# Kernel tuning notes

Measured on AMD Instinct MI355X. Metric: run time of the kernel, lower is better.

## Reference

```python
import jax, jax.numpy as jnp
import numpy as np

B, T, C, H = 2, 2048, 1024, 16
HD = C // H  # head dim = 64


def setup_inputs() -> dict:
    key = jax.random.key(0)
    k1, k2, k3 = jax.random.split(key, 3)
    x = jax.random.normal(k1, (B, T, C), dtype=jnp.float32)
    W_attn = jax.random.normal(k2, (C, 3 * C), dtype=jnp.float32) * (C ** -0.5)
    W_proj = jax.random.normal(k3, (C, C), dtype=jnp.float32) * (C ** -0.5)
    b_proj = jnp.zeros((C,), dtype=jnp.float32)
    return {"x": x, "W_attn": W_attn, "W_proj": W_proj, "b_proj": b_proj}


def reference(x, W_attn, W_proj, b_proj):
    Bv, Tv, Cv = x.shape
    qkv = x @ W_attn  # [B, T, 3C]  (no bias: config.bias=False)
    # NOTE: source splits as k, q, v (k first!)
    k, q, v = jnp.split(qkv, 3, axis=2)
    # [B, H, T, HD]
    q = q.reshape(Bv, Tv, H, HD).transpose(0, 2, 1, 3)
    k = k.reshape(Bv, Tv, H, HD).transpose(0, 2, 1, 3)
    v = v.reshape(Bv, Tv, H, HD).transpose(0, 2, 1, 3)
    wei = jnp.einsum('bhqd,bhkd->bhqk', q, k) * (HD ** -0.5)
    causal = jnp.tril(jnp.ones((Tv, Tv), dtype=bool))
    wei = jnp.where(causal, wei, -jnp.inf)
    wei = jax.nn.softmax(wei, axis=-1)
    # dropout = 0.0 (eval) -> identity
    out = jnp.einsum('bhqk,bhkd->bhqd', wei, v)
    out = out.transpose(0, 2, 1, 3).reshape(Bv, Tv, Cv)
    out = out @ W_proj + b_proj
    return out
```

## Files before the change

### kernel.cpp

```cpp
#include <hip/hip_runtime.h>

typedef __attribute__((ext_vector_type(8))) short short8;
typedef __attribute__((ext_vector_type(4))) short short4v;
typedef __attribute__((ext_vector_type(4))) float float4v;

#define T_SEQ 2048
#define CDIM 1024
#define NHEAD 16
#define HDIM 64
#define LROW 40
#define PROW 72

__device__ __forceinline__ unsigned short f2bf(float f) {
    unsigned u = __builtin_bit_cast(unsigned, f);
    u += 0x7FFF + ((u >> 16) & 1);
    return (unsigned short)(u >> 16);
}

__global__ __launch_bounds__(256) void convert_f32_bf16_vec(
    const float* __restrict__ in, unsigned short* __restrict__ out) {
    int i = blockIdx.x * 256 + threadIdx.x;
    float4 v = ((const float4*)in)[i];
    ushort4 o;
    o.x = f2bf(v.x); o.y = f2bf(v.y); o.z = f2bf(v.z); o.w = f2bf(v.w);
    ((ushort4*)out)[i] = o;
}

__global__ __launch_bounds__(256) void transpose_f32_bf16(
    const float* __restrict__ in, unsigned short* __restrict__ out, int K, int N) {
    __shared__ float tile[32][33];
    int kb = blockIdx.x * 32, nb = blockIdx.y * 32;
    int tx = threadIdx.x & 31, ty = threadIdx.x >> 5;
    for (int r = 0; r < 4; r++)
        tile[ty + r * 8][tx] = in[(size_t)(kb + ty + r * 8) * N + nb + tx];
    __syncthreads();
    for (int r = 0; r < 4; r++)
        out[(size_t)(nb + ty + r * 8) * K + kb + tx] = f2bf(tile[tx][ty + r * 8]);
}

__global__ __launch_bounds__(256) void gemm_qkv(
    const unsigned short* __restrict__ A, const unsigned short* __restrict__ Bt,
    unsigned short* __restrict__ dK, unsigned short* __restrict__ dQ,
    unsigned short* __restrict__ dV) {
    const int K = 1024;
    const int NITER = K / 32;
    __shared__ unsigned short sA[2][128 * LROW];
    __shared__ unsigned short sB[2][128 * LROW];
    int tid = threadIdx.x, wave = tid >> 6, lane = tid & 63;
    int quad = lane >> 4, l16 = lane & 15;
    int wm = wave >> 1, wn = wave & 1;
    int blockM = blockIdx.y * 128, blockN = blockIdx.x * 128;
    int rlane = lane >> 2, seg = lane & 3;
    bool swapAB = (blockN >= 2048);

    const unsigned short* gA = A + (size_t)blockM * K;
    const unsigned short* gB = Bt + (size_t)blockN * K;

    float4v acc[4][4] = {};
    uint4 ra[2], rb[2];

    int srow[2], soff[2];
    for (int i = 0; i < 2; i++) {
        srow[i] = wave * 32 + i * 16 + rlane;
        soff[i] = srow[i] * LROW + seg * 8;
    }

    for (int i = 0; i < 2; i++) {
        ra[i] = *(const uint4*)(gA + (size_t)srow[i] * K + seg * 8);
        rb[i] = *(const uint4*)(gB + (size_t)srow[i] * K + seg * 8);
    }
    for (int i = 0; i < 2; i++) {
        *(uint4*)(sA[0] + soff[i]) = ra[i];
        *(uint4*)(sB[0] + soff[i]) = rb[i];
    }

    int aoff = (wm * 64 + l16) * LROW + quad * 8;
    int boff = (wn * 64 + l16) * LROW + quad * 8;

    for (int it = 0; it < NITER; it++) {
        int cur = it & 1;
        __syncthreads();
        if (it + 1 < NITER) {
            int kb = (it + 1) * 32;
            for (int i = 0; i < 2; i++) {
                ra[i] = *(const uint4*)(gA + (size_t)srow[i] * K + kb + seg * 8);
                rb[i] = *(const uint4*)(gB + (size_t)srow[i] * K + kb + seg * 8);
            }
        }
        const unsigned short* cA = sA[cur];
        const unsigned short* cB = sB[cur];
        short8 af[4], bf[4];
        for (int i = 0; i < 4; i++)
            af[i] = *(const short8*)(cA + aoff + i * 16 * LROW);
        for (int j = 0; j < 4; j++)
            bf[j] = *(const short8*)(cB + boff + j * 16 * LROW);
        if (!swapAB) {
            for (int i = 0; i < 4; i++)
                for (int j = 0; j < 4; j++)
                    acc[i][j] = __builtin_amdgcn_mfma_f32_16x16x32_bf16(
                        af[i], bf[j], acc[i][j], 0, 0, 0);
        } else {
            for (int i = 0; i < 4; i++)
                for (int j = 0; j < 4; j++)
                    acc[i][j] = __builtin_amdgcn_mfma_f32_16x16x32_bf16(
                        bf[j], af[i], acc[i][j], 0, 0, 0);
        }
        if (it + 1 < NITER) {
            int nxt = cur ^ 1;
            for (int i = 0; i < 2; i++) {
                *(uint4*)(sA[nxt] + soff[i]) = ra[i];
                *(uint4*)(sB[nxt] + soff[i]) = rb[i];
            }
        }
    }

    if (!swapAB) {
        const float QSCL = 0.18033688011112042f;
        for (int i = 0; i < 4; i++)
            for (int j = 0; j < 4; j++)
                for (int r = 0; r < 4; r++) {
                    int m = blockM + wm * 64 + i * 16 + quad * 4 + r;
                    int n = blockN + wn * 64 + j * 16 + l16;
                    int part = n >> 10, c = n & 1023;
                    int h = c >> 6, d = c & 63;
                    int bb = m >> 11, t = m & 2047;
                    int bh = bb * NHEAD + h;
                    if (part == 0) {
                        dK[(((size_t)bh * T_SEQ + t) << 6) + d] = f2bf(acc[i][j][r]);
                    } else {
                        dQ[(((size_t)bh * T_SEQ + t) << 6) + d] =
                            f2bf(acc[i][j][r] * QSCL);
                    }
                }
    } else {
        for (int i = 0; i < 4; i++)
            for (int j = 0; j < 4; j++)
                for (int r = 0; r < 4; r++) {
                    int n = blockN + wn * 64 + j * 16 + quad * 4 + r;
                    int m = blockM + wm * 64 + i * 16 + l16;
                    int c = n & 1023;
                    int h = c >> 6, d = c & 63;
                    int bb = m >> 11, t = m & 2047;
                    int bh = bb * NHEAD + h;
                    dV[((size_t)bh * HDIM + d) * T_SEQ + t] = f2bf(acc[i][j][r]);
                }
    }
}

__global__ __launch_bounds__(256) void gemm_proj(
    const unsigned short* __restrict__ A, const unsigned short* __restrict__ Bt,
    const float* __restrict__ bias, float* __restrict__ out) {
    const int K = 1024;
    const int NITER = K / 64;
    __shared__ unsigned short sA[2][64 * PROW];
    __shared__ unsigned short sB[2][64 * PROW];
    int tid = threadIdx.x, wave = tid >> 6, lane = tid & 63;
    int quad = lane >> 4, l16 = lane & 15;
    int wm = wave >> 1, wn = wave & 1;
    int blockM = blockIdx.y * 64, blockN = blockIdx.x * 64;

    int srow = tid >> 3;
    int sseg = tid & 7;
    const unsigned short* gA0 = A + (size_t)(blockM + srow) * K + sseg * 8;
    const unsigned short* gA1 = gA0 + (size_t)32 * K;
    const unsigned short* gB0 = Bt + (size_t)(blockN + srow) * K + sseg * 8;
    const unsigned short* gB1 = gB0 + (size_t)32 * K;
    int so0 = srow * PROW + sseg * 8;
    int so1 = (srow + 32) * PROW + sseg * 8;

    float4v acc[2][2] = {};
    uint4 ra0, ra1, rb0, rb1;

    ra0 = *(const uint4*)gA0; ra1 = *(const uint4*)gA1;
    rb0 = *(const uint4*)gB0; rb1 = *(const uint4*)gB1;
    *(uint4*)(sA[0] + so0) = ra0;
    *(uint4*)(sA[0] + so1) = ra1;
    *(uint4*)(sB[0] + so0) = rb0;
    *(uint4*)(sB[0] + so1) = rb1;

    int aoff = (wm * 32 + l16) * PROW + quad * 8;
    int boff = (wn * 32 + l16) * PROW + quad * 8;

    for (int it = 0; it < NITER; it++) {
        int cur = it & 1;
        __syncthreads();
        if (it + 1 < NITER) {
            int kb = (it + 1) * 64;
            ra0 = *(const uint4*)(gA0 + kb); ra1 = *(const uint4*)(gA1 + kb);
            rb0 = *(const uint4*)(gB0 + kb); rb1 = *(const uint4*)(gB1 + kb);
        }
        const unsigned short* cA = sA[cur];
        const unsigned short* cB = sB[cur];
        short8 af[2][2], bf[2][2];
        for (int i = 0; i < 2; i++)
            for (int k = 0; k < 2; k++)
                af[i][k] = *(const short8*)(cA + aoff + i * 16 * PROW + k * 32);
        for (int j = 0; j < 2; j++)
            for (int k = 0; k < 2; k++)
                bf[j][k] = *(const short8*)(cB + boff + j * 16 * PROW + k * 32);
        for (int i = 0; i < 2; i++)
            for (int j = 0; j < 2; j++) {
                acc[i][j] = __builtin_amdgcn_mfma_f32_16x16x32_bf16(
                    af[i][0], bf[j][0], acc[i][j], 0, 0, 0);
                acc[i][j] = __builtin_amdgcn_mfma_f32_16x16x32_bf16(
                    af[i][1], bf[j][1], acc[i][j], 0, 0, 0);
            }
        if (it + 1 < NITER) {
            int nxt = cur ^ 1;
            *(uint4*)(sA[nxt] + so0) = ra0;
            *(uint4*)(sA[nxt] + so1) = ra1;
            *(uint4*)(sB[nxt] + so0) = rb0;
            *(uint4*)(sB[nxt] + so1) = rb1;
        }
    }

    for (int i = 0; i < 2; i++)
        for (int j = 0; j < 2; j++)
            for (int r = 0; r < 4; r++) {
                int m = blockM + wm * 32 + i * 16 + quad * 4 + r;
                int n = blockN + wn * 32 + j * 16 + l16;
                out[(size_t)m * CDIM + n] = acc[i][j][r] + bias[n];
            }
}

__global__ __launch_bounds__(256) void attn_fwd(
    const unsigned short* __restrict__ Qp, const unsigned short* __restrict__ Kp,
    const unsigned short* __restrict__ Vt, unsigned short* __restrict__ att) {
    __shared__ unsigned short sK[2][64 * 72];
    __shared__ unsigned short sV[2][64 * 72];
    int tid = threadIdx.x, wave = tid >> 6, lane = tid & 63;
    int quad = lane >> 4, l16 = lane & 15;
    int bh = blockIdx.x;
    int bb = bh >> 4, h = bh & 15;
    size_t baseQ = (size_t)bh * T_SEQ * HDIM;
    size_t baseV = (size_t)bh * HDIM * T_SEQ;
    int row4 = tid >> 2, seg = tid & 3;

    int xt = 31 - blockIdx.y;
    int qb = xt * 64;
    int qrow = qb + wave * 16 + l16;

    const unsigned short* qr = Qp + baseQ + (size_t)qrow * HDIM;
    short8 qf0 = *(const short8*)(qr + quad * 8);
    short8 qf1 = *(const short8*)(qr + 32 + quad * 8);

    float4v o[4] = {};
    float lsum = 0.f;
    int nt = xt + 1;

    uint4 ka, kb2, va, vb;
    {
        const unsigned short* gk = Kp + baseQ + (size_t)row4 * HDIM + seg * 16;
        const unsigned short* gv = Vt + baseV + (size_t)row4 * T_SEQ + seg * 16;
        ka = *(const uint4*)gk; kb2 = *(const uint4*)(gk + 8);
        va = *(const uint4*)gv; vb = *(const uint4*)(gv + 8);
    }
    *(uint4*)(sK[0] + row4 * 72 + seg * 16) = ka;
    *(uint4*)(sK[0] + row4 * 72 + seg * 16 + 8) = kb2;
    *(uint4*)(sV[0] + row4 * 72 + seg * 16) = va;
    *(uint4*)(sV[0] + row4 * 72 + seg * 16 + 8) = vb;

    for (int t = 0; t < nt; t++) {
        int cur = t & 1;
        __syncthreads();
        if (t + 1 < nt) {
            const unsigned short* gk =
                Kp + baseQ + (size_t)((t + 1) * 64 + row4) * HDIM + seg * 16;
            const unsigned short* gv =
                Vt + baseV + (size_t)row4 * T_SEQ + (t + 1) * 64 + seg * 16;
            ka = *(const uint4*)gk; kb2 = *(const uint4*)(gk + 8);
            va = *(const uint4*)gv; vb = *(const uint4*)(gv + 8);
        }

        const unsigned short* cK = sK[cur];
        const unsigned short* cV = sV[cur];
        float4v s[4];
        for (int sub = 0; sub < 4; sub++) {
            short8 kf0 = *(const short8*)(cK + (sub * 16 + l16) * 72 + quad * 8);
            short8 kf1 =
                *(const short8*)(cK + (sub * 16 + l16) * 72 + 32 + quad * 8);
            float4v z = {};
            z = __builtin_amdgcn_mfma_f32_16x16x32_bf16(kf0, qf0, z, 0, 0, 0);
            z = __builtin_amdgcn_mfma_f32_16x16x32_bf16(kf1, qf1, z, 0, 0, 0);
            s[sub] = z;
        }

        bool need_mask = (t * 64 + 63) > (qb + wave * 16);
        float p[16];
        for (int sub = 0; sub < 4; sub++)
            for (int r = 0; r < 4; r++) {
                float v = s[sub][r];
                if (need_mask) {
                    int kg = t * 64 + sub * 16 + quad * 4 + r;
                    v = (kg <= qrow) ? v : -1e30f;
                }
                p[sub * 4 + r] = v;
            }
        unsigned ub[16];
        for (int i = 0; i < 16; i++) {
            float e = exp2f(p[i] - 16.0f);
            unsigned u = __builtin_bit_cast(unsigned, e) & 0xffff0000u;
            ub[i] = u;
            lsum += __builtin_bit_cast(float, u);
        }

        for (int sub = 0; sub < 4; sub++) {
            unsigned lo = __builtin_amdgcn_perm(ub[sub * 4 + 1], ub[sub * 4 + 0],
                                                0x07060302u);
            unsigned hi = __builtin_amdgcn_perm(ub[sub * 4 + 3], ub[sub * 4 + 2],
                                                0x07060302u);
            uint2 packed = {lo, hi};
            short4v pf = __builtin_bit_cast(short4v, packed);
            for (int dc = 0; dc < 4; dc++) {
                short4v vf = *(const short4v*)(
                    cV + (dc * 16 + l16) * 72 + sub * 16 + quad * 4);
                o[dc] = __builtin_amdgcn_mfma_f32_16x16x16bf16_1k(
                    vf, pf, o[dc], 0, 0, 0);
            }
        }

        if (t + 1 < nt) {
            int nxt = cur ^ 1;
            *(uint4*)(sK[nxt] + row4 * 72 + seg * 16) = ka;
            *(uint4*)(sK[nxt] + row4 * 72 + seg * 16 + 8) = kb2;
            *(uint4*)(sV[nxt] + row4 * 72 + seg * 16) = va;
            *(uint4*)(sV[nxt] + row4 * 72 + seg * 16 + 8) = vb;
        }
    }

    lsum += __shfl_xor(lsum, 16);
    lsum += __shfl_xor(lsum, 32);
    float inv = 1.0f / lsum;

    __syncthreads();
    for (int dc = 0; dc < 4; dc++) {
        short4v ov;
        for (int r = 0; r < 4; r++) ov[r] = (short)f2bf(o[dc][r] * inv);
        *(short4v*)(sK[0] + wave * 1152 + l16 * 72 + dc * 16 + quad * 4) = ov;
    }
    __syncthreads();
    int orow = lane >> 2, oseg = lane & 3;
    uint4 a = *(const uint4*)(sK[0] + wave * 1152 + orow * 72 + oseg * 16);
    uint4 b = *(const uint4*)(sK[0] + wave * 1152 + orow * 72 + oseg * 16 + 8);
    unsigned short* dst = att +
        (size_t)(bb * T_SEQ + qb + wave * 16 + orow) * CDIM + h * HDIM +
        oseg * 16;
    *(uint4*)dst = a;
    *(uint4*)(dst + 8) = b;
}

extern "C" void kernel_launch(void* const* d_in, const int* in_sizes, int n_in,
                              void* d_out, int out_size, void* d_ws, size_t ws_size,
                              hipStream_t stream) {
    const float* x      = (const float*)d_in[0];
    const float* W_attn = (const float*)d_in[1];
    const float* W_proj = (const float*)d_in[2];
    const float* b_proj = (const float*)d_in[3];
    float* out = (float*)d_out;

    unsigned short* xb   = (unsigned short*)d_ws;
    unsigned short* WaT  = xb  + 4096 * 1024;
    unsigned short* WpT  = WaT + 3072 * 1024;
    unsigned short* Karr = WpT + 1024 * 1024;
    unsigned short* Qarr = Karr + 2 * 16 * 2048 * 64;
    unsigned short* Varr = Qarr + 2 * 16 * 2048 * 64;
    unsigned short* attb = Varr + 2 * 16 * 2048 * 64;

    convert_f32_bf16_vec<<<4096, 256, 0, stream>>>(x, xb);
    transpose_f32_bf16<<<dim3(32, 96), 256, 0, stream>>>(W_attn, WaT, 1024, 3072);
    transpose_f32_bf16<<<dim3(32, 32), 256, 0, stream>>>(W_proj, WpT, 1024, 1024);
    gemm_qkv<<<dim3(24, 32), 256, 0, stream>>>(xb, WaT, Karr, Qarr, Varr);
    attn_fwd<<<dim3(32, 32), 256, 0, stream>>>(Qarr, Karr, Varr, attb);
    gemm_proj<<<dim3(16, 64), 256, 0, stream>>>(attb, WpT, b_proj, out);
}
```

Before: 199.8 us.

## Load QKV GEMM tiles directly into LDS with global_load_lds

Replaces the register-staged, double-buffered global-to-LDS copy in the QKV GEMM with direct global_load_lds 16-byte transfers into a single unpadded LDS buffer. Each k-step now issues its loads, syncs, computes, and syncs again. This removes register staging and the ds_write instructions, and halves LDS use. In exchange it loses the load/compute overlap of double buffering and drops the row padding, which may cause LDS bank conflicts on the fragment reads.

```diff
diff --git a/kernel.cpp b/kernel.cpp
--- a/kernel.cpp
+++ b/kernel.cpp
@@ -8,13 +8,19 @@
 #define CDIM 1024
 #define NHEAD 16
 #define HDIM 64
-#define LROW 40
 #define PROW 72
 
 __device__ __forceinline__ unsigned short f2bf(float f) {
     unsigned u = __builtin_bit_cast(unsigned, f);
     u += 0x7FFF + ((u >> 16) & 1);
     return (unsigned short)(u >> 16);
+}
+
+__device__ __forceinline__ void gload16(const unsigned short* g,
+                                        unsigned short* l) {
+    __builtin_amdgcn_global_load_lds(
+        (const __attribute__((address_space(1))) unsigned int*)g,
+        (__attribute__((address_space(3))) unsigned int*)l, 16, 0, 0);
 }
 
 __global__ __launch_bounds__(256) void convert_f32_bf16_vec(
@@ -43,57 +49,43 @@
     unsigned short* __restrict__ dK, unsigned short* __restrict__ dQ,
     unsigned short* __restrict__ dV) {
     const int K = 1024;
-    const int NITER = K / 32;
-    __shared__ unsigned short sA[2][128 * LROW];
-    __shared__ unsigned short sB[2][128 * LROW];
+    __shared__ unsigned short sA[128 * 32];
+    __shared__ unsigned short sB[128 * 32];
     int tid = threadIdx.x, wave = tid >> 6, lane = tid & 63;
     int quad = lane >> 4, l16 = lane & 15;
     int wm = wave >> 1, wn = wave & 1;
     int blockM = blockIdx.y * 128, blockN = blockIdx.x * 128;
-    int rlane = lane >> 2, seg = lane & 3;
     bool swapAB = (blockN >= 2048);
 
     const unsigned short* gA = A + (size_t)blockM * K;
     const unsigned short* gB = Bt + (size_t)blockN * K;
 
+    int srow = wave * 32 + (lane >> 2);
+    int scol = (lane & 3) * 8;
+    const unsigned short* pa0 = gA + (size_t)srow * K + scol;
+    const unsigned short* pa1 = pa0 + (size_t)16 * K;
+    const unsigned short* pb0 = gB + (size_t)srow * K + scol;
+    const unsigned short* pb1 = pb0 + (size_t)16 * K;
+    unsigned short* la0 = sA + (wave * 32) * 32;
+    unsigned short* la1 = sA + (wave * 32 + 16) * 32;
+    unsigned short* lb0 = sB + (wave * 32) * 32;
+    unsigned short* lb1 = sB + (wave * 32 + 16) * 32;
+
     float4v acc[4][4] = {};
-    uint4 ra[2], rb[2];
-
-    int srow[2], soff[2];
-    for (int i = 0; i < 2; i++) {
-        srow[i] = wave * 32 + i * 16 + rlane;
-        soff[i] = srow[i] * LROW + seg * 8;
-    }
-
-    for (int i = 0; i < 2; i++) {
-        ra[i] = *(const uint4*)(gA + (size_t)srow[i] * K + seg * 8);
-        rb[i] = *(const uint4*)(gB + (size_t)srow[i] * K + seg * 8);
-    }
-    for (int i = 0; i < 2; i++) {
-        *(uint4*)(sA[0] + soff[i]) = ra[i];
-        *(uint4*)(sB[0] + soff[i]) = rb[i];
-    }
-
-    int aoff = (wm * 64 + l16) * LROW + quad * 8;
-    int boff = (wn * 64 + l16) * LROW + quad * 8;
-
-    for (int it = 0; it < NITER; it++) {
-        int cur = it & 1;
+    int aoff = (wm * 64 + l16) * 32 + quad * 8;
+    int boff = (wn * 64 + l16) * 32 + quad * 8;
+
+    for (int kb = 0; kb < K; kb += 32) {
+        gload16(pa0 + kb, la0);
+        gload16(pa1 + kb, la1);
+        gload16(pb0 + kb, lb0);
+        gload16(pb1 + kb, lb1);
         __syncthreads();
-        if (it + 1 < NITER) {
-            int kb = (it + 1) * 32;
-            for (int i = 0; i < 2; i++) {
-                ra[i] = *(const uint4*)(gA + (size_t)srow[i] * K + kb + seg * 8);
-                rb[i] = *(const uint4*)(gB + (size_t)srow[i] * K + kb + seg * 8);
-            }
-        }
-        const unsigned short* cA = sA[cur];
-        const unsigned short* cB = sB[cur];
         short8 af[4], bf[4];
         for (int i = 0; i < 4; i++)
-            af[i] = *(const short8*)(cA + aoff + i * 16 * LROW);
+            af[i] = *(const short8*)(sA + aoff + i * 16 * 32);
         for (int j = 0; j < 4; j++)
-            bf[j] = *(const short8*)(cB + boff + j * 16 * LROW);
+            bf[j] = *(const short8*)(sB + boff + j * 16 * 32);
         if (!swapAB) {
             for (int i = 0; i < 4; i++)
                 for (int j = 0; j < 4; j++)
@@ -105,13 +97,7 @@
                     acc[i][j] = __builtin_amdgcn_mfma_f32_16x16x32_bf16(
                         bf[j], af[i], acc[i][j], 0, 0, 0);
         }
-        if (it + 1 < NITER) {
-            int nxt = cur ^ 1;
-            for (int i = 0; i < 2; i++) {
-                *(uint4*)(sA[nxt] + soff[i]) = ra[i];
-                *(uint4*)(sB[nxt] + soff[i]) = rb[i];
-            }
-        }
+        __syncthreads();
     }
 
     if (!swapAB) {
```

Result: slower. 210.2 us (+5.2%).
